# Kernel tuning notes

Hardware: AMD Instinct MI355X
Metric: run time of the kernel (lower is better)

Reference implementation:

```python
import jax, jax.numpy as jnp
import numpy as np

LAMBDA_TEMPORAL = 0.5
LAMBDA_IDENTITY = 0.1
EPS = 1e-6


def setup_inputs() -> dict:
    key = jax.random.key(0)
    k1, k2, k3 = jax.random.split(key, 3)
    B, T, N = 16, 256, 2048
    pred_tracks_3d = jax.random.normal(k1, (B, T, N, 3), dtype=jnp.float32)
    gt_tracks_3d = jax.random.normal(k2, (B, T, N, 3), dtype=jnp.float32)
    gt_visibility = jax.random.uniform(k3, (B, T, N), dtype=jnp.float32)
    return {
        'pred_tracks_3d': pred_tracks_3d,
        'gt_tracks_3d': gt_tracks_3d,
        'gt_visibility': gt_visibility,
    }


def _compute_losses(pred, gt, vis):
    # visibility mask (B, T, N)
    m = (vis > 0.5).astype(pred.dtype)
    num_visible = jnp.sum(m)

    coord_w = jnp.array([1.0, 1.0, 2.0], dtype=pred.dtype)
    weighted_sq = jnp.square(pred - gt) * coord_w  # (B,T,N,3)
    recon = jnp.where(
        num_visible > 0,
        jnp.sum(weighted_sq * m[..., None]) / jnp.maximum(num_visible, 1.0),
        0.0,
    )

    # --- temporal: masked velocity MSE (visible in both adjacent frames) ---
    pred_vel = pred[:, 1:] - pred[:, :-1]
    gt_vel = gt[:, 1:] - gt[:, :-1]
    vel_mask = m[:, 1:] * m[:, :-1]  # (B,T-1,N)
    num_vel = jnp.sum(vel_mask)
    temporal = jnp.where(
        num_vel > 0,
        jnp.sum(jnp.square(pred_vel - gt_vel) * vel_mask[..., None]) / jnp.maximum(num_vel, 1.0),
        0.0,
    )

    # --- identity: per-point unbiased variance ratio over visible (b,t) samples ---
    n = jnp.sum(m, axis=(0, 1))  # (N,) visible count per point

    def masked_var(x):
        # unbiased (ddof=1) per-point, per-coord variance over masked (B,T) entries
        mean = jnp.einsum('btn,btnc->nc', m, x) / jnp.maximum(n, 1.0)[:, None]
        ss = jnp.einsum('btn,btnc->nc', m, jnp.square(x - mean[None, None]))
        return ss / jnp.maximum(n - 1.0, 1.0)[:, None]  # (N,3)

    pred_var = masked_var(pred)
    gt_var = masked_var(gt)
    var_ratio = jnp.sum(jnp.abs(pred_var - gt_var), axis=1) / (jnp.sum(gt_var, axis=1) + EPS)
    num_points = pred.shape[2]
    identity = jnp.sum(jnp.where(n > 1, var_ratio, 0.0)) / num_points

    # --- adaptive re-weighting (no-grad in original) ---
    rl = jax.lax.stop_gradient(recon)
    tl = jax.lax.stop_gradient(temporal)
    il = jax.lax.stop_gradient(identity)
    all_pos = (rl > 0) & (tl > 0) & (il > 0)
    max_comp = jnp.maximum(jnp.maximum(rl, tl), il)
    target = max_comp / 3.0
    thresh = 10.0 * target

    def adjust(base, comp):
        return jnp.where(all_pos & (comp > thresh), base * target / jnp.maximum(comp, 1e-30), base)

    rec_w = adjust(1.0, rl)
    temp_w = adjust(LAMBDA_TEMPORAL, tl)
    id_w = adjust(LAMBDA_IDENTITY, il)

    total = rec_w * recon + temp_w * temporal + id_w * identity
    return jnp.stack([total, recon, temporal, identity])


def reference(pred_tracks_3d, gt_tracks_3d, gt_visibility):
    # returns [total_loss, reconstruction_loss, temporal_loss, identity_loss]
    return _compute_losses(pred_tracks_3d, gt_tracks_3d, gt_visibility)
```

## Files before the change

### kernel.cpp

```cpp
#include <hip/hip_runtime.h>

#define BB 16
#define TT 256
#define NN 2048
#define TC 16
#define NSLICE 8
#define WSBASE 16


__device__ __forceinline__ float waveReduceSum(float v) {
#pragma unroll
  for (int o = 32; o > 0; o >>= 1) v += __shfl_down(v, o, 64);
  return v;
}

__global__ __launch_bounds__(256, 8) void stats_kernel(
    const float* __restrict__ pred, const float* __restrict__ gt,
    const float* __restrict__ vis, float* __restrict__ ws) {
  const int n  = blockIdx.x * 256 + threadIdx.x;
  const int b  = blockIdx.y;
  const int t0 = blockIdx.z * TC;

  const size_t frame0 = (size_t)(b * TT + t0) * NN + n;
  const float3* __restrict__ pp = (const float3*)pred + frame0;
  const float3* __restrict__ gp = (const float3*)gt + frame0;
  const float*  __restrict__ vp = vis + frame0;

  float cnt = 0.f;
  float sp0 = 0, sp1 = 0, sp2 = 0, qp0 = 0, qp1 = 0, qp2 = 0;
  float sg0 = 0, sg1 = 0, sg2 = 0, qg0 = 0, qg1 = 0, qg2 = 0;
  float recon = 0, temporal = 0, nvel = 0;

  float3 ppv, pgv;
  float mprev;
  {
    const long off = (t0 == 0) ? 0 : -(long)NN;
    ppv = pp[off];
    pgv = gp[off];
    float v = vp[off];
    mprev = (t0 != 0 && v > 0.5f) ? 1.f : 0.f;
  }

#pragma unroll
  for (int i = 0; i < TC; ++i) {
    float3 a = pp[(size_t)i * NN];
    float3 g = gp[(size_t)i * NN];
    float v = vp[(size_t)i * NN];
    float m = (v > 0.5f) ? 1.f : 0.f;

    cnt += m;
    sp0 += m * a.x; sp1 += m * a.y; sp2 += m * a.z;
    qp0 += m * a.x * a.x; qp1 += m * a.y * a.y; qp2 += m * a.z * a.z;
    sg0 += m * g.x; sg1 += m * g.y; sg2 += m * g.z;
    qg0 += m * g.x * g.x; qg1 += m * g.y * g.y; qg2 += m * g.z * g.z;
    float d0 = a.x - g.x, d1 = a.y - g.y, d2 = a.z - g.z;
    recon += m * (d0 * d0 + d1 * d1 + 2.f * d2 * d2);

    float mv = m * mprev;
    float vx = (a.x - ppv.x) - (g.x - pgv.x);
    float vy = (a.y - ppv.y) - (g.y - pgv.y);
    float vz = (a.z - ppv.z) - (g.z - pgv.z);
    temporal += mv * (vx * vx + vy * vy + vz * vz);
    nvel += mv;

    ppv = a; pgv = g; mprev = m;
  }

  float* pts = ws + WSBASE + (size_t)(b & (NSLICE - 1)) * 13 * NN;
  atomicAdd(&pts[0 * NN + n], cnt);
  atomicAdd(&pts[1 * NN + n], sp0);
  atomicAdd(&pts[2 * NN + n], sp1);
  atomicAdd(&pts[3 * NN + n], sp2);
  atomicAdd(&pts[4 * NN + n], qp0);
  atomicAdd(&pts[5 * NN + n], qp1);
  atomicAdd(&pts[6 * NN + n], qp2);
  atomicAdd(&pts[7 * NN + n], sg0);
  atomicAdd(&pts[8 * NN + n], sg1);
  atomicAdd(&pts[9 * NN + n], sg2);
  atomicAdd(&pts[10 * NN + n], qg0);
  atomicAdd(&pts[11 * NN + n], qg1);
  atomicAdd(&pts[12 * NN + n], qg2);

  __shared__ float sred[3][4];
  float r0 = waveReduceSum(recon);
  float r1 = waveReduceSum(temporal);
  float r2 = waveReduceSum(nvel);
  int lane = threadIdx.x & 63, w = threadIdx.x >> 6;
  if (lane == 0) { sred[0][w] = r0; sred[1][w] = r1; sred[2][w] = r2; }
  __syncthreads();
  if (threadIdx.x < 3) {
    float s = sred[threadIdx.x][0] + sred[threadIdx.x][1] +
              sred[threadIdx.x][2] + sred[threadIdx.x][3];
    atomicAdd(&ws[threadIdx.x], s);
  }
}

__global__ __launch_bounds__(256) void identity_kernel(float* __restrict__ ws) {
  const int n = blockIdx.x * 256 + threadIdx.x;
  const float* base = ws + WSBASE;
  float st[13];
#pragma unroll
  for (int k = 0; k < 13; ++k) st[k] = 0.f;
#pragma unroll
  for (int s = 0; s < NSLICE; ++s) {
    const float* pts = base + (size_t)s * 13 * NN;
#pragma unroll
    for (int k = 0; k < 13; ++k) st[k] += pts[k * NN + n];
  }
  float c = st[0];
  float sp0 = st[1], sp1 = st[2], sp2 = st[3];
  float qp0 = st[4], qp1 = st[5], qp2 = st[6];
  float sg0 = st[7], sg1 = st[8], sg2 = st[9];
  float qg0 = st[10], qg1 = st[11], qg2 = st[12];

  float inv = 1.f / fmaxf(c, 1.f);
  float dv  = 1.f / fmaxf(c - 1.f, 1.f);
  float pv0 = (qp0 - sp0 * sp0 * inv) * dv;
  float pv1 = (qp1 - sp1 * sp1 * inv) * dv;
  float pv2 = (qp2 - sp2 * sp2 * inv) * dv;
  float gv0 = (qg0 - sg0 * sg0 * inv) * dv;
  float gv1 = (qg1 - sg1 * sg1 * inv) * dv;
  float gv2 = (qg2 - sg2 * sg2 * inv) * dv;

  float num = fabsf(pv0 - gv0) + fabsf(pv1 - gv1) + fabsf(pv2 - gv2);
  float den = gv0 + gv1 + gv2 + 1e-6f;
  float contrib = (c > 1.f) ? (num / den) : 0.f;

  __shared__ float sred[2][4];
  float r0 = waveReduceSum(contrib);
  float r1 = waveReduceSum(c);
  int lane = threadIdx.x & 63, w = threadIdx.x >> 6;
  if (lane == 0) { sred[0][w] = r0; sred[1][w] = r1; }
  __syncthreads();
  if (threadIdx.x < 2) {
    float s = sred[threadIdx.x][0] + sred[threadIdx.x][1] +
              sred[threadIdx.x][2] + sred[threadIdx.x][3];
    atomicAdd(&ws[3 + threadIdx.x], s);
  }
}

__global__ void finalize_kernel(const float* __restrict__ ws, float* __restrict__ out) {
  float nv = ws[4];
  float recon = (nv > 0.f) ? ws[0] / fmaxf(nv, 1.f) : 0.f;
  float nvel = ws[2];
  float temporal = (nvel > 0.f) ? ws[1] / fmaxf(nvel, 1.f) : 0.f;
  float identity = ws[3] / (float)NN;

  float rl = recon, tl = temporal, il = identity;
  bool all_pos = (rl > 0.f) && (tl > 0.f) && (il > 0.f);
  float maxc = fmaxf(rl, fmaxf(tl, il));
  float target = maxc / 3.f;
  float thresh = 10.f * target;
  float rw = (all_pos && rl > thresh) ? 1.0f * target / fmaxf(rl, 1e-30f) : 1.0f;
  float tw = (all_pos && tl > thresh) ? 0.5f * target / fmaxf(tl, 1e-30f) : 0.5f;
  float iw = (all_pos && il > thresh) ? 0.1f * target / fmaxf(il, 1e-30f) : 0.1f;

  out[0] = rw * recon + tw * temporal + iw * identity;
  out[1] = recon;
  out[2] = temporal;
  out[3] = identity;
}

extern "C" void kernel_launch(void* const* d_in, const int* in_sizes, int n_in,
                              void* d_out, int out_size, void* d_ws, size_t ws_size,
                              hipStream_t stream) {
  const float* pred = (const float*)d_in[0];
  const float* gt   = (const float*)d_in[1];
  const float* vis  = (const float*)d_in[2];
  float* out = (float*)d_out;
  float* ws  = (float*)d_ws;

  hipMemsetAsync(d_ws, 0, (WSBASE + (size_t)NSLICE * 13 * NN) * sizeof(float), stream);

  dim3 g1(NN / 256, BB, TT / TC);
  stats_kernel<<<g1, 256, 0, stream>>>(pred, gt, vis, ws);
  identity_kernel<<<dim3(NN / 256), 256, 0, stream>>>(ws);
  finalize_kernel<<<1, 1, 0, stream>>>(ws, out);
}
```

Measured before the change: 254.4 us.

## Vectorize stats loads with float4 per-thread point groups and LDS pre-reduction

Each thread now handles 4 consecutive points, loading pred/gt/vis with 128-bit float4 loads instead of float3 and scalar loads. Each of the four waves in a block takes an 8-frame sub-chunk of a 32-frame block. Per-point statistics are combined in shared memory before the global atomics, and the atomics are spread over 16 slices, including the scalar recon/temporal sums. The aim is wider memory transactions and less contention on global atomics. In exchange, register pressure rises (52 accumulators per thread, launch bounds cut to 3 blocks/SM), there are LDS atomics, and the first frame of each sub-chunk is reloaded.

```diff
diff --git a/kernel.cpp b/kernel.cpp
--- a/kernel.cpp
+++ b/kernel.cpp
@@ -3,9 +3,10 @@
 #define BB 16
 #define TT 256
 #define NN 2048
-#define TC 16
-#define NSLICE 8
-#define WSBASE 16
+#define CT 32
+#define TI 8
+#define NSLICE 16
+#define WSBASE 64
 
 
 __device__ __forceinline__ float waveReduceSum(float v) {
@@ -14,84 +15,119 @@
   return v;
 }
 
-__global__ __launch_bounds__(256, 8) void stats_kernel(
+__global__ __launch_bounds__(256, 3) void stats_kernel(
     const float* __restrict__ pred, const float* __restrict__ gt,
     const float* __restrict__ vis, float* __restrict__ ws) {
-  const int n  = blockIdx.x * 256 + threadIdx.x;
-  const int b  = blockIdx.y;
-  const int t0 = blockIdx.z * TC;
-
-  const size_t frame0 = (size_t)(b * TT + t0) * NN + n;
-  const float3* __restrict__ pp = (const float3*)pred + frame0;
-  const float3* __restrict__ gp = (const float3*)gt + frame0;
-  const float*  __restrict__ vp = vis + frame0;
-
-  float cnt = 0.f;
-  float sp0 = 0, sp1 = 0, sp2 = 0, qp0 = 0, qp1 = 0, qp2 = 0;
-  float sg0 = 0, sg1 = 0, sg2 = 0, qg0 = 0, qg1 = 0, qg2 = 0;
-  float recon = 0, temporal = 0, nvel = 0;
-
-  float3 ppv, pgv;
-  float mprev;
+  const int tid  = threadIdx.x;
+  const int lane = tid & 63;
+  const int team = tid >> 6;
+  const int nb   = blockIdx.x * 256;
+  const int n0   = nb + lane * 4;
+  const int b    = blockIdx.y;
+  const int tf   = blockIdx.z * CT + team * TI;
+
+  const size_t rowe = (size_t)NN * 3;
+  const float* __restrict__ pbase = pred + ((size_t)(b * TT + tf) * NN + n0) * 3;
+  const float* __restrict__ gbase = gt   + ((size_t)(b * TT + tf) * NN + n0) * 3;
+  const float* __restrict__ vbase = vis  + (size_t)(b * TT + tf) * NN + n0;
+
+  float acc[4][13];
+#pragma unroll
+  for (int j = 0; j < 4; ++j)
+#pragma unroll
+    for (int k = 0; k < 13; ++k) acc[j][k] = 0.f;
+  float pv[4][3], gv[4][3], mp[4];
+  float recon = 0.f, temporal = 0.f, nvel = 0.f;
+
   {
-    const long off = (t0 == 0) ? 0 : -(long)NN;
-    ppv = pp[off];
-    pgv = gp[off];
-    float v = vp[off];
-    mprev = (t0 != 0 && v > 0.5f) ? 1.f : 0.f;
-  }
-
-#pragma unroll
-  for (int i = 0; i < TC; ++i) {
-    float3 a = pp[(size_t)i * NN];
-    float3 g = gp[(size_t)i * NN];
-    float v = vp[(size_t)i * NN];
-    float m = (v > 0.5f) ? 1.f : 0.f;
-
-    cnt += m;
-    sp0 += m * a.x; sp1 += m * a.y; sp2 += m * a.z;
-    qp0 += m * a.x * a.x; qp1 += m * a.y * a.y; qp2 += m * a.z * a.z;
-    sg0 += m * g.x; sg1 += m * g.y; sg2 += m * g.z;
-    qg0 += m * g.x * g.x; qg1 += m * g.y * g.y; qg2 += m * g.z * g.z;
-    float d0 = a.x - g.x, d1 = a.y - g.y, d2 = a.z - g.z;
-    recon += m * (d0 * d0 + d1 * d1 + 2.f * d2 * d2);
-
-    float mv = m * mprev;
-    float vx = (a.x - ppv.x) - (g.x - pgv.x);
-    float vy = (a.y - ppv.y) - (g.y - pgv.y);
-    float vz = (a.z - ppv.z) - (g.z - pgv.z);
-    temporal += mv * (vx * vx + vy * vy + vz * vz);
-    nvel += mv;
-
-    ppv = a; pgv = g; mprev = m;
-  }
-
-  float* pts = ws + WSBASE + (size_t)(b & (NSLICE - 1)) * 13 * NN;
-  atomicAdd(&pts[0 * NN + n], cnt);
-  atomicAdd(&pts[1 * NN + n], sp0);
-  atomicAdd(&pts[2 * NN + n], sp1);
-  atomicAdd(&pts[3 * NN + n], sp2);
-  atomicAdd(&pts[4 * NN + n], qp0);
-  atomicAdd(&pts[5 * NN + n], qp1);
-  atomicAdd(&pts[6 * NN + n], qp2);
-  atomicAdd(&pts[7 * NN + n], sg0);
-  atomicAdd(&pts[8 * NN + n], sg1);
-  atomicAdd(&pts[9 * NN + n], sg2);
-  atomicAdd(&pts[10 * NN + n], qg0);
-  atomicAdd(&pts[11 * NN + n], qg1);
-  atomicAdd(&pts[12 * NN + n], qg2);
+    const long off  = (tf == 0) ? 0 : -(long)rowe;
+    const long voff = (tf == 0) ? 0 : -(long)NN;
+    float4 A = *(const float4*)(pbase + off);
+    float4 Bv = *(const float4*)(pbase + off + 4);
+    float4 Cv = *(const float4*)(pbase + off + 8);
+    float4 D = *(const float4*)(gbase + off);
+    float4 E = *(const float4*)(gbase + off + 4);
+    float4 F = *(const float4*)(gbase + off + 8);
+    float4 V = *(const float4*)(vbase + voff);
+    float ap[12] = {A.x,A.y,A.z,A.w,Bv.x,Bv.y,Bv.z,Bv.w,Cv.x,Cv.y,Cv.z,Cv.w};
+    float ag[12] = {D.x,D.y,D.z,D.w,E.x,E.y,E.z,E.w,F.x,F.y,F.z,F.w};
+    float av[4]  = {V.x,V.y,V.z,V.w};
+#pragma unroll
+    for (int j = 0; j < 4; ++j) {
+      pv[j][0] = ap[3*j]; pv[j][1] = ap[3*j+1]; pv[j][2] = ap[3*j+2];
+      gv[j][0] = ag[3*j]; gv[j][1] = ag[3*j+1]; gv[j][2] = ag[3*j+2];
+      mp[j] = (tf != 0 && av[j] > 0.5f) ? 1.f : 0.f;
+    }
+  }
+
+#pragma unroll
+  for (int i = 0; i < TI; ++i) {
+    const float* p = pbase + (size_t)i * rowe;
+    const float* g = gbase + (size_t)i * rowe;
+    const float* v = vbase + (size_t)i * NN;
+    float4 A = *(const float4*)(p);
+    float4 Bv = *(const float4*)(p + 4);
+    float4 Cv = *(const float4*)(p + 8);
+    float4 D = *(const float4*)(g);
+    float4 E = *(const float4*)(g + 4);
+    float4 F = *(const float4*)(g + 8);
+    float4 V = *(const float4*)(v);
+    float ap[12] = {A.x,A.y,A.z,A.w,Bv.x,Bv.y,Bv.z,Bv.w,Cv.x,Cv.y,Cv.z,Cv.w};
+    float ag[12] = {D.x,D.y,D.z,D.w,E.x,E.y,E.z,E.w,F.x,F.y,F.z,F.w};
+    float av[4]  = {V.x,V.y,V.z,V.w};
+
+#pragma unroll
+    for (int j = 0; j < 4; ++j) {
+      float x  = ap[3*j], y  = ap[3*j+1], z  = ap[3*j+2];
+      float gx = ag[3*j], gy = ag[3*j+1], gz = ag[3*j+2];
+      float m = (av[j] > 0.5f) ? 1.f : 0.f;
+      acc[j][0]  += m;
+      acc[j][1]  += m * x;      acc[j][2]  += m * y;      acc[j][3]  += m * z;
+      acc[j][4]  += m * x * x;  acc[j][5]  += m * y * y;  acc[j][6]  += m * z * z;
+      acc[j][7]  += m * gx;     acc[j][8]  += m * gy;     acc[j][9]  += m * gz;
+      acc[j][10] += m * gx * gx; acc[j][11] += m * gy * gy; acc[j][12] += m * gz * gz;
+      float d0 = x - gx, d1 = y - gy, d2 = z - gz;
+      recon += m * (d0 * d0 + d1 * d1 + 2.f * d2 * d2);
+      float mv = m * mp[j];
+      float vx = (x - pv[j][0]) - (gx - gv[j][0]);
+      float vy = (y - pv[j][1]) - (gy - gv[j][1]);
+      float vz = (z - pv[j][2]) - (gz - gv[j][2]);
+      temporal += mv * (vx * vx + vy * vy + vz * vz);
+      nvel += mv;
+      pv[j][0] = x;  pv[j][1] = y;  pv[j][2] = z;
+      gv[j][0] = gx; gv[j][1] = gy; gv[j][2] = gz;
+      mp[j] = m;
+    }
+  }
+
+  __shared__ float lacc[13][256];
+#pragma unroll
+  for (int k = 0; k < 13; ++k) lacc[k][tid] = 0.f;
+  __syncthreads();
+#pragma unroll
+  for (int j = 0; j < 4; ++j) {
+    const int col = lane | (j << 6);
+#pragma unroll
+    for (int k = 0; k < 13; ++k) atomicAdd(&lacc[k][col], acc[j][k]);
+  }
+  __syncthreads();
+
+  const int slice = (b + 2 * blockIdx.z) & (NSLICE - 1);
+  float* pts = ws + WSBASE + (size_t)slice * 13 * NN;
+  const int swz = (tid >> 2) | ((tid & 3) << 6);
+#pragma unroll
+  for (int k = 0; k < 13; ++k)
+    atomicAdd(&pts[(size_t)k * NN + nb + tid], lacc[k][swz]);
 
   __shared__ float sred[3][4];
   float r0 = waveReduceSum(recon);
   float r1 = waveReduceSum(temporal);
   float r2 = waveReduceSum(nvel);
-  int lane = threadIdx.x & 63, w = threadIdx.x >> 6;
-  if (lane == 0) { sred[0][w] = r0; sred[1][w] = r1; sred[2][w] = r2; }
-  __syncthreads();
-  if (threadIdx.x < 3) {
-    float s = sred[threadIdx.x][0] + sred[threadIdx.x][1] +
-              sred[threadIdx.x][2] + sred[threadIdx.x][3];
-    atomicAdd(&ws[threadIdx.x], s);
+  if (lane == 0) { sred[0][team] = r0; sred[1][team] = r1; sred[2][team] = r2; }
+  __syncthreads();
+  if (tid < 3) {
+    float s = sred[tid][0] + sred[tid][1] + sred[tid][2] + sred[tid][3];
+    atomicAdd(&ws[slice * 3 + tid], s);
   }
 }
 
@@ -103,9 +139,8 @@
   for (int k = 0; k < 13; ++k) st[k] = 0.f;
 #pragma unroll
   for (int s = 0; s < NSLICE; ++s) {
-    const float* pts = base + (size_t)s * 13 * NN;
-#pragma unroll
-    for (int k = 0; k < 13; ++k) st[k] += pts[k * NN + n];
+#pragma unroll
+    for (int k = 0; k < 13; ++k) st[k] += base[(size_t)(s * 13 + k) * NN + n];
   }
   float c = st[0];
   float sp0 = st[1], sp1 = st[2], sp2 = st[3];
@@ -135,30 +170,41 @@
   if (threadIdx.x < 2) {
     float s = sred[threadIdx.x][0] + sred[threadIdx.x][1] +
               sred[threadIdx.x][2] + sred[threadIdx.x][3];
-    atomicAdd(&ws[3 + threadIdx.x], s);
+    atomicAdd(&ws[48 + threadIdx.x], s);
   }
 }
 
 __global__ void finalize_kernel(const float* __restrict__ ws, float* __restrict__ out) {
-  float nv = ws[4];
-  float recon = (nv > 0.f) ? ws[0] / fmaxf(nv, 1.f) : 0.f;
-  float nvel = ws[2];
-  float temporal = (nvel > 0.f) ? ws[1] / fmaxf(nvel, 1.f) : 0.f;
-  float identity = ws[3] / (float)NN;
-
-  float rl = recon, tl = temporal, il = identity;
-  bool all_pos = (rl > 0.f) && (tl > 0.f) && (il > 0.f);
-  float maxc = fmaxf(rl, fmaxf(tl, il));
-  float target = maxc / 3.f;
-  float thresh = 10.f * target;
-  float rw = (all_pos && rl > thresh) ? 1.0f * target / fmaxf(rl, 1e-30f) : 1.0f;
-  float tw = (all_pos && tl > thresh) ? 0.5f * target / fmaxf(tl, 1e-30f) : 0.5f;
-  float iw = (all_pos && il > thresh) ? 0.1f * target / fmaxf(il, 1e-30f) : 0.1f;
-
-  out[0] = rw * recon + tw * temporal + iw * identity;
-  out[1] = recon;
-  out[2] = temporal;
-  out[3] = identity;
+  const int lane = threadIdx.x;
+  float r = 0.f, t = 0.f, v = 0.f;
+  if (lane < NSLICE) {
+    r = ws[lane * 3 + 0];
+    t = ws[lane * 3 + 1];
+    v = ws[lane * 3 + 2];
+  }
+  r = waveReduceSum(r);
+  t = waveReduceSum(t);
+  v = waveReduceSum(v);
+  if (lane == 0) {
+    float nvis = ws[49];
+    float recon = (nvis > 0.f) ? r / fmaxf(nvis, 1.f) : 0.f;
+    float temporal = (v > 0.f) ? t / fmaxf(v, 1.f) : 0.f;
+    float identity = ws[48] / (float)NN;
+
+    float rl = recon, tl = temporal, il = identity;
+    bool all_pos = (rl > 0.f) && (tl > 0.f) && (il > 0.f);
+    float maxc = fmaxf(rl, fmaxf(tl, il));
+    float target = maxc / 3.f;
+    float thresh = 10.f * target;
+    float rw = (all_pos && rl > thresh) ? 1.0f * target / fmaxf(rl, 1e-30f) : 1.0f;
+    float tw = (all_pos && tl > thresh) ? 0.5f * target / fmaxf(tl, 1e-30f) : 0.5f;
+    float iw = (all_pos && il > thresh) ? 0.1f * target / fmaxf(il, 1e-30f) : 0.1f;
+
+    out[0] = rw * recon + tw * temporal + iw * identity;
+    out[1] = recon;
+    out[2] = temporal;
+    out[3] = identity;
+  }
 }
 
 extern "C" void kernel_launch(void* const* d_in, const int* in_sizes, int n_in,
@@ -172,8 +218,8 @@
 
   hipMemsetAsync(d_ws, 0, (WSBASE + (size_t)NSLICE * 13 * NN) * sizeof(float), stream);
 
-  dim3 g1(NN / 256, BB, TT / TC);
+  dim3 g1(NN / 256, BB, TT / CT);
   stats_kernel<<<g1, 256, 0, stream>>>(pred, gt, vis, ws);
   identity_kernel<<<dim3(NN / 256), 256, 0, stream>>>(ws);
-  finalize_kernel<<<1, 1, 0, stream>>>(ws, out);
-}
+  finalize_kernel<<<1, 64, 0, stream>>>(ws, out);
+}
```

New measurement: 294.4 us. 1.16x slower.
